# Kernel tuning notes

Measured on AMD Instinct MI355X. Metric: run time of the kernel, lower is better.

## Reference

```python
import jax, jax.numpy as jnp
import numpy as np

N_EMBED = 1024
HEAD_SIZE = 64


def setup_inputs() -> dict:
    key = jax.random.key(0)
    kx, kq, kk, kv = jax.random.split(key, 4)
    x = jax.random.normal(kx, (8, 2048, N_EMBED), dtype=jnp.float32)
    s = 1.0 / np.sqrt(N_EMBED)
    # nn.Linear weights are [out, in]; store as [in, out] for x @ W
    W_q = jax.random.uniform(kq, (N_EMBED, HEAD_SIZE), jnp.float32, -s, s)
    W_k = jax.random.uniform(kk, (N_EMBED, HEAD_SIZE), jnp.float32, -s, s)
    W_v = jax.random.uniform(kv, (N_EMBED, HEAD_SIZE), jnp.float32, -s, s)
    return {"x": x, "W_q": W_q, "W_k": W_k, "W_v": W_v}


def reference(x, W_q, W_k, W_v):
    b, t, c = x.shape
    q = x @ W_q  # [b, t, h]
    k = x @ W_k
    v = x @ W_v
    scale = k.shape[-1] ** -0.5
    wei = jnp.einsum("bqh,bkh->bqk", q, k) * scale  # [b, t, t]
    causal = jnp.tril(jnp.ones((t, t), dtype=bool))
    wei = jnp.where(causal, wei, -jnp.inf)
    wei = jax.nn.softmax(wei, axis=-1)
    # dropout p=0.0 -> identity
    return jnp.einsum("bqk,bkh->bqh", wei, v)
```

## Files before the change

kernel.cpp:

```cpp
#include <hip/hip_runtime.h>
#include <math.h>

typedef unsigned short u16;
typedef unsigned int u32;
typedef __attribute__((ext_vector_type(4))) float f32x4;
typedef __attribute__((ext_vector_type(8))) short s16x8;
typedef __attribute__((ext_vector_type(4))) unsigned short u16x4;

#define T_ 2048
#define C_ 1024

__device__ __forceinline__ u16 f2b(float f) {
  u32 u = __builtin_bit_cast(u32, f);
  return (u16)((u + 0x8000u) >> 16);
}

__device__ __forceinline__ s16x8 pack8v(f32x4 a, f32x4 b) {
  s16x8 r;
  r[0] = (short)f2b(a[0]); r[1] = (short)f2b(a[1]);
  r[2] = (short)f2b(a[2]); r[3] = (short)f2b(a[3]);
  r[4] = (short)f2b(b[0]); r[5] = (short)f2b(b[1]);
  r[6] = (short)f2b(b[2]); r[7] = (short)f2b(b[3]);
  return r;
}

__device__ __forceinline__ void gld_lds16(const void* g, void* l) {
  __builtin_amdgcn_global_load_lds(
      (const __attribute__((address_space(1))) u32*)g,
      (__attribute__((address_space(3))) u32*)l, 16, 0, 0);
}

__global__ __launch_bounds__(256) void wconv(const float* __restrict__ Wq,
                                             const float* __restrict__ Wk,
                                             const float* __restrict__ Wv,
                                             u16* __restrict__ Wt) {
  __shared__ u16 t[64][68];
  const int bm = blockIdx.x >> 4;
  const int kt = blockIdx.x & 15;
  const float* src = (bm == 0) ? Wq : ((bm == 1) ? Wk : Wv);
  const float scale = (bm == 0) ? 0.18033688f : 1.0f;
  const int krow = threadIdx.x >> 2;
  const int c0 = (threadIdx.x & 3) * 16;
  const float* sp = src + (size_t)(kt * 64 + krow) * 64 + c0;
#pragma unroll
  for (int i = 0; i < 4; ++i) {
    float4 v = *(const float4*)(sp + i * 4);
    t[c0 + i * 4 + 0][krow] = f2b(v.x * scale);
    t[c0 + i * 4 + 1][krow] = f2b(v.y * scale);
    t[c0 + i * 4 + 2][krow] = f2b(v.z * scale);
    t[c0 + i * 4 + 3][krow] = f2b(v.w * scale);
  }
  __syncthreads();
  const int n = threadIdx.x >> 2;
  const int koff = (threadIdx.x & 3) * 16;
  u16* dst = Wt + (size_t)(bm * 64 + n) * C_ + kt * 64 + koff;
#pragma unroll
  for (int i = 0; i < 4; ++i)
    *(u16x4*)(dst + i * 4) = *(const u16x4*)(&t[n][koff + i * 4]);
}

__global__ __launch_bounds__(256, 2) void proj(const float* __restrict__ x,
                                               const u16* __restrict__ Wt,
                                               u16* __restrict__ qo,
                                               u16* __restrict__ ko,
                                               u16* __restrict__ vt) {
  __shared__ __align__(16) float xs[32 * 64];
  __shared__ __align__(16) u16 wsh[192 * 64];
  const int tid = threadIdx.x;
  const int wave = tid >> 6, lane = tid & 63;
  const int quad = lane >> 4, l15 = lane & 15;
  const int mg = wave >> 1, nh = wave & 1;
  const int m0 = blockIdx.x * 32;

  const int xrow_in = lane >> 4;
  const int xslot = lane & 15;
  const int wrow_in = lane >> 3;
  const int wg = (lane & 7) ^ wrow_in;

  f32x4 acc[6];
#pragma unroll
  for (int j = 0; j < 6; ++j) acc[j] = {0.f, 0.f, 0.f, 0.f};

  for (int kt = 0; kt < 16; ++kt) {
#pragma unroll
    for (int c = 0; c < 2; ++c) {
      const int row = 8 * wave + 4 * c + xrow_in;
      const int g = xslot ^ (row & 15);
      gld_lds16(x + (size_t)(m0 + row) * C_ + kt * 64 + g * 4,
                &xs[(8 * wave + 4 * c) * 64]);
    }
#pragma unroll
    for (int c = 0; c < 6; ++c) {
      const int row = (6 * wave + c) * 8 + wrow_in;
      gld_lds16(Wt + (size_t)row * C_ + kt * 64 + wg * 8,
                &wsh[(6 * wave + c) * 8 * 64]);
    }
    __syncthreads();
    s16x8 af[2];
#pragma unroll
    for (int ks = 0; ks < 2; ++ks) {
      const int row = 16 * mg + l15;
      const int cc = ks * 8 + quad * 2;
      f32x4 p0 = *(const f32x4*)&xs[row * 64 + ((cc ^ (row & 15)) * 4)];
      f32x4 p1 = *(const f32x4*)&xs[row * 64 + (((cc + 1) ^ (row & 15)) * 4)];
      af[ks] = pack8v(p0, p1);
    }
#pragma unroll
    for (int jj = 0; jj < 6; ++jj) {
      const int row = (nh * 6 + jj) * 16 + l15;
#pragma unroll
      for (int ks = 0; ks < 2; ++ks) {
        const int cc = ks * 4 + quad;
        s16x8 bf = *(const s16x8*)&wsh[row * 64 + ((cc ^ (row & 7)) * 8)];
        acc[jj] = __builtin_amdgcn_mfma_f32_16x16x32_bf16(af[ks], bf, acc[jj], 0, 0, 0);
      }
    }
    __syncthreads();
  }

  const int r0 = m0 + 16 * mg + quad * 4;
#pragma unroll
  for (int jj = 0; jj < 6; ++jj) {
    const int ns = nh * 6 + jj;
    if (ns < 4) {
      const int col = ns * 16 + l15;
#pragma unroll
      for (int i = 0; i < 4; ++i)
        qo[(size_t)(r0 + i) * 64 + col] = f2b(acc[jj][i]);
    } else if (ns < 8) {
      const int col = (ns - 4) * 16 + l15;
#pragma unroll
      for (int i = 0; i < 4; ++i)
        ko[(size_t)(r0 + i) * 64 + col] = f2b(acc[jj][i]);
    } else {
      const int d = (ns - 8) * 16 + l15;
      const int bb = r0 >> 11, t0 = r0 & 2047;
      u16x4 pk = {f2b(acc[jj][0]), f2b(acc[jj][1]), f2b(acc[jj][2]), f2b(acc[jj][3])};
      *(u16x4*)(vt + (size_t)bb * (64 * T_) + (size_t)d * T_ + t0) = pk;
    }
  }
}

__global__ __launch_bounds__(256, 4) void attn(const u16* __restrict__ qw,
                                               const u16* __restrict__ kw,
                                               const u16* __restrict__ vt,
                                               float* __restrict__ out) {
  __shared__ __align__(16) u16 Pb[4][16 * 72];
  __shared__ float mbuf[4][16];
  __shared__ float lbuf[4][16];
  const int tid = threadIdx.x;
  const int wave = tid >> 6, lane = tid & 63;
  const int quad = lane >> 4, l15 = lane & 15;
  const int b = blockIdx.x & 7;
  const int qt = 127 - (blockIdx.x >> 3);

  const u16* qp = qw + ((size_t)b * T_ + qt * 16) * 64;
  const u16* kb = kw + (size_t)b * T_ * 64;
  const u16* vb = vt + (size_t)b * 64 * T_;

  s16x8 qf[2];
#pragma unroll
  for (int ks = 0; ks < 2; ++ks)
    qf[ks] = *(const s16x8*)(qp + l15 * 64 + ks * 32 + quad * 8);

  f32x4 o[4];
#pragma unroll
  for (int m = 0; m < 4; ++m) o[m] = {0.f, 0.f, 0.f, 0.f};
  float mr = -INFINITY, lr = 0.0f;

  u16* P = Pb[wave];
  const int jd = qt >> 2;

  for (int j = wave; j <= jd; j += 4) {
    const u16* kp = kb + (size_t)j * 64 * 64;
    const u16* vp = vb + j * 64;
    s16x8 kf[2][4], vf[2][4];
#pragma unroll
    for (int ks = 0; ks < 2; ++ks)
#pragma unroll
      for (int m = 0; m < 4; ++m)
        kf[ks][m] = *(const s16x8*)(kp + (16 * m + l15) * 64 + ks * 32 + quad * 8);
#pragma unroll
    for (int ks = 0; ks < 2; ++ks)
#pragma unroll
      for (int m = 0; m < 4; ++m)
        vf[ks][m] = *(const s16x8*)(vp + (size_t)(16 * m + l15) * T_ + ks * 32 + quad * 8);

    f32x4 s[4];
#pragma unroll
    for (int m = 0; m < 4; ++m) s[m] = {0.f, 0.f, 0.f, 0.f};
#pragma unroll
    for (int ks = 0; ks < 2; ++ks)
#pragma unroll
      for (int m = 0; m < 4; ++m)
        s[m] = __builtin_amdgcn_mfma_f32_16x16x32_bf16(kf[ks][m], qf[ks], s[m], 0, 0, 0);

    if (j == jd) {
#pragma unroll
      for (int m = 0; m < 4; ++m)
#pragma unroll
        for (int i = 0; i < 4; ++i)
          if (64 * jd + 16 * m + quad * 4 + i > 16 * qt + l15) s[m][i] = -INFINITY;
    }
    float mt = s[0][0];
#pragma unroll
    for (int m = 0; m < 4; ++m)
#pragma unroll
      for (int i = 0; i < 4; ++i) mt = fmaxf(mt, s[m][i]);
    mt = fmaxf(mt, __shfl_xor(mt, 16));
    mt = fmaxf(mt, __shfl_xor(mt, 32));
    const float mn = fmaxf(mr, mt);
    const float al = exp2f(mr - mn);
    mr = mn;
    float rs = 0.0f;
#pragma unroll
    for (int m = 0; m < 4; ++m)
#pragma unroll
      for (int i = 0; i < 4; ++i) {
        float p = exp2f(s[m][i] - mn);
        s[m][i] = p;
        rs += p;
      }
    rs += __shfl_xor(rs, 16);
    rs += __shfl_xor(rs, 32);
    lr = lr * al + rs;
#pragma unroll
    for (int m = 0; m < 4; ++m) {
      u16x4 pk = {f2b(s[m][0]), f2b(s[m][1]), f2b(s[m][2]), f2b(s[m][3])};
      *(u16x4*)(&P[l15 * 72 + 16 * m + quad * 4]) = pk;
    }
#pragma unroll
    for (int m = 0; m < 4; ++m) o[m] *= al;
#pragma unroll
    for (int ks = 0; ks < 2; ++ks) {
      s16x8 pf = *(const s16x8*)(&P[l15 * 72 + ks * 32 + quad * 8]);
#pragma unroll
      for (int m = 0; m < 4; ++m)
        o[m] = __builtin_amdgcn_mfma_f32_16x16x32_bf16(vf[ks][m], pf, o[m], 0, 0, 0);
    }
  }
  if (quad == 0) {
    mbuf[wave][l15] = mr;
    lbuf[wave][l15] = lr;
  }
#pragma unroll
  for (int m = 0; m < 4; ++m) {
    u16x4 pk = {f2b(o[m][0]), f2b(o[m][1]), f2b(o[m][2]), f2b(o[m][3])};
    *(u16x4*)(&Pb[wave][l15 * 72 + 16 * m + quad * 4]) = pk;
  }
  __syncthreads();
  const int r = tid >> 4;
  const int cg = (tid & 15) * 4;
  float fw[4];
  float mstar = -INFINITY, lsum = 0.0f;
#pragma unroll
  for (int w = 0; w < 4; ++w) mstar = fmaxf(mstar, mbuf[w][r]);
#pragma unroll
  for (int w = 0; w < 4; ++w) {
    fw[w] = exp2f(mbuf[w][r] - mstar);
    lsum += fw[w] * lbuf[w][r];
  }
  const float inv = 1.0f / lsum;
  float a0 = 0.f, a1 = 0.f, a2 = 0.f, a3 = 0.f;
#pragma unroll
  for (int w = 0; w < 4; ++w) {
    u16x4 vv = *(const u16x4*)(&Pb[w][r * 72 + cg]);
    a0 += fw[w] * __builtin_bit_cast(float, ((u32)vv[0]) << 16);
    a1 += fw[w] * __builtin_bit_cast(float, ((u32)vv[1]) << 16);
    a2 += fw[w] * __builtin_bit_cast(float, ((u32)vv[2]) << 16);
    a3 += fw[w] * __builtin_bit_cast(float, ((u32)vv[3]) << 16);
  }
  float4 st = {a0 * inv, a1 * inv, a2 * inv, a3 * inv};
  *(float4*)(out + ((size_t)b * T_ + qt * 16 + r) * 64 + cg) = st;
}

extern "C" void kernel_launch(void* const* d_in, const int* in_sizes, int n_in,
                              void* d_out, int out_size, void* d_ws, size_t ws_size,
                              hipStream_t stream) {
  const float* x  = (const float*)d_in[0];
  const float* Wq = (const float*)d_in[1];
  const float* Wk = (const float*)d_in[2];
  const float* Wv = (const float*)d_in[3];
  float* out = (float*)d_out;
  char* ws = (char*)d_ws;
  u16* Wt = (u16*)ws;
  u16* q  = (u16*)(ws + 393216);
  u16* k  = (u16*)(ws + 393216 + 2097152);
  u16* vT = (u16*)(ws + 393216 + 2 * 2097152);
  hipLaunchKernelGGL(wconv, dim3(48), dim3(256), 0, stream, Wq, Wk, Wv, Wt);
  hipLaunchKernelGGL(proj, dim3(512), dim3(256), 0, stream, x, Wt, q, k, vT);
  hipLaunchKernelGGL(attn, dim3(1024), dim3(256), 0, stream, q, k, vT, out);
}
```

Before: 151.8 us.

## Widen projection K-tile to 128 and prefetch next K fragments in attention

```diff
diff --git a/kernel.cpp b/kernel.cpp
--- a/kernel.cpp
+++ b/kernel.cpp
@@ -64,54 +64,55 @@
                                                u16* __restrict__ qo,
                                                u16* __restrict__ ko,
                                                u16* __restrict__ vt) {
-  __shared__ __align__(16) float xs[32 * 64];
-  __shared__ __align__(16) u16 wsh[192 * 64];
+  __shared__ __align__(16) u32 smem[16384];
+  float* xs = (float*)smem;
+  u16* wsh = (u16*)(smem + 4096);
   const int tid = threadIdx.x;
   const int wave = tid >> 6, lane = tid & 63;
   const int quad = lane >> 4, l15 = lane & 15;
   const int mg = wave >> 1, nh = wave & 1;
   const int m0 = blockIdx.x * 32;
 
-  const int xrow_in = lane >> 4;
-  const int xslot = lane & 15;
-  const int wrow_in = lane >> 3;
-  const int wg = (lane & 7) ^ wrow_in;
+  const int xslot = lane & 31, xrin = lane >> 5;
+  const int wslot = lane & 15, wrin = lane >> 4;
 
   f32x4 acc[6];
 #pragma unroll
   for (int j = 0; j < 6; ++j) acc[j] = {0.f, 0.f, 0.f, 0.f};
 
-  for (int kt = 0; kt < 16; ++kt) {
-#pragma unroll
-    for (int c = 0; c < 2; ++c) {
-      const int row = 8 * wave + 4 * c + xrow_in;
-      const int g = xslot ^ (row & 15);
-      gld_lds16(x + (size_t)(m0 + row) * C_ + kt * 64 + g * 4,
-                &xs[(8 * wave + 4 * c) * 64]);
-    }
-#pragma unroll
-    for (int c = 0; c < 6; ++c) {
-      const int row = (6 * wave + c) * 8 + wrow_in;
-      gld_lds16(Wt + (size_t)row * C_ + kt * 64 + wg * 8,
-                &wsh[(6 * wave + c) * 8 * 64]);
+  for (int kt = 0; kt < 8; ++kt) {
+    const int k0 = kt * 128;
+#pragma unroll
+    for (int c = 0; c < 4; ++c) {
+      const int row = wave * 8 + c * 2 + xrin;
+      const int g = xslot ^ (row & 31);
+      gld_lds16(x + (size_t)(m0 + row) * C_ + k0 + g * 4,
+                &xs[(wave * 8 + c * 2) * 128]);
+    }
+#pragma unroll
+    for (int c = 0; c < 12; ++c) {
+      const int row = (wave * 12 + c) * 4 + wrin;
+      const int g = wslot ^ (row & 15);
+      gld_lds16(Wt + (size_t)row * C_ + k0 + g * 8,
+                &wsh[(wave * 12 + c) * 4 * 128]);
     }
     __syncthreads();
-    s16x8 af[2];
-#pragma unroll
-    for (int ks = 0; ks < 2; ++ks) {
-      const int row = 16 * mg + l15;
+    const int r = 16 * mg + l15;
+    s16x8 af[4];
+#pragma unroll
+    for (int ks = 0; ks < 4; ++ks) {
       const int cc = ks * 8 + quad * 2;
-      f32x4 p0 = *(const f32x4*)&xs[row * 64 + ((cc ^ (row & 15)) * 4)];
-      f32x4 p1 = *(const f32x4*)&xs[row * 64 + (((cc + 1) ^ (row & 15)) * 4)];
+      f32x4 p0 = *(const f32x4*)&xs[r * 128 + ((cc ^ (r & 31)) * 4)];
+      f32x4 p1 = *(const f32x4*)&xs[r * 128 + (((cc + 1) ^ (r & 31)) * 4)];
       af[ks] = pack8v(p0, p1);
     }
 #pragma unroll
     for (int jj = 0; jj < 6; ++jj) {
-      const int row = (nh * 6 + jj) * 16 + l15;
-#pragma unroll
-      for (int ks = 0; ks < 2; ++ks) {
+      const int R = (nh * 6 + jj) * 16 + l15;
+#pragma unroll
+      for (int ks = 0; ks < 4; ++ks) {
         const int cc = ks * 4 + quad;
-        s16x8 bf = *(const s16x8*)&wsh[row * 64 + ((cc ^ (row & 7)) * 8)];
+        s16x8 bf = *(const s16x8*)&wsh[R * 128 + ((cc ^ (R & 15)) * 8)];
         acc[jj] = __builtin_amdgcn_mfma_f32_16x16x32_bf16(af[ks], bf, acc[jj], 0, 0, 0);
       }
     }
@@ -171,29 +172,43 @@
   u16* P = Pb[wave];
   const int jd = qt >> 2;
 
+  s16x8 kf[2][4];
+  if (wave <= jd) {
+    const u16* kp = kb + (size_t)wave * 64 * 64;
+#pragma unroll
+    for (int ks = 0; ks < 2; ++ks)
+#pragma unroll
+      for (int m = 0; m < 4; ++m)
+        kf[ks][m] = *(const s16x8*)(kp + (16 * m + l15) * 64 + ks * 32 + quad * 8);
+  }
+
   for (int j = wave; j <= jd; j += 4) {
-    const u16* kp = kb + (size_t)j * 64 * 64;
     const u16* vp = vb + j * 64;
-    s16x8 kf[2][4], vf[2][4];
+    s16x8 vf[2][4];
 #pragma unroll
     for (int ks = 0; ks < 2; ++ks)
 #pragma unroll
       for (int m = 0; m < 4; ++m)
-        kf[ks][m] = *(const s16x8*)(kp + (16 * m + l15) * 64 + ks * 32 + quad * 8);
+        vf[ks][m] = *(const s16x8*)(vp + (size_t)(16 * m + l15) * T_ + ks * 32 + quad * 8);
+
+    f32x4 s[4];
+#pragma unroll
+    for (int m = 0; m < 4; ++m) s[m] = {0.f, 0.f, 0.f, 0.f};
 #pragma unroll
     for (int ks = 0; ks < 2; ++ks)
 #pragma unroll
       for (int m = 0; m < 4; ++m)
-        vf[ks][m] = *(const s16x8*)(vp + (size_t)(16 * m + l15) * T_ + ks * 32 + quad * 8);
-
-    f32x4 s[4];
-#pragma unroll
-    for (int m = 0; m < 4; ++m) s[m] = {0.f, 0.f, 0.f, 0.f};
-#pragma unroll
-    for (int ks = 0; ks < 2; ++ks)
-#pragma unroll
-      for (int m = 0; m < 4; ++m)
         s[m] = __builtin_amdgcn_mfma_f32_16x16x32_bf16(kf[ks][m], qf[ks], s[m], 0, 0, 0);
+
+    {
+      const int jn = (j + 4 <= jd) ? j + 4 : jd;
+      const u16* kp = kb + (size_t)jn * 64 * 64;
+#pragma unroll
+      for (int ks = 0; ks < 2; ++ks)
+#pragma unroll
+        for (int m = 0; m < 4; ++m)
+          kf[ks][m] = *(const s16x8*)(kp + (16 * m + l15) * 64 + ks * 32 + quad * 8);
+    }
 
     if (j == jd) {
 #pragma unroll
```

Result: slower. 168.8 us (+11.1%).
